# Kernel optimization log

Measured on AMD Instinct MI355X. Metric: run time of the kernel, lower is better.

Reference implementation:

```python
import jax, jax.numpy as jnp
import numpy as np


def setup_inputs() -> dict:
    key = jax.random.key(0)
    k1, k2, k3, k4, k5 = jax.random.split(key, 5)
    B, N, D, H = 4, 1024, 128, 64
    return {
        "embeddings": jax.random.normal(k1, (B, N, D), dtype=jnp.float32),
        "W1": jax.random.normal(k2, (2 * D, H), dtype=jnp.float32) * 0.05,  # Linear(2D -> 64), x@W layout
        "b1": jax.random.normal(k3, (H,), dtype=jnp.float32) * 0.05,
        "W2": jax.random.normal(k4, (H, 1), dtype=jnp.float32) * 0.05,      # Linear(64 -> 1)
        "b2": jax.random.normal(k5, (1,), dtype=jnp.float32) * 0.05,
    }


def reference(embeddings, W1, b1, W2, b2):
    # Original: cat([e_i, e_j]) @ W1 == e_i @ W1[:D] + e_j @ W1[D:]
    # so we compute per-node projections and broadcast-sum, never forming
    # the (B,N,N,2D) concat tensor. Same math, far less traffic.
    B, N, D = embeddings.shape
    Wa, Wb = W1[:D], W1[D:]                      # each (D, 64)
    h_i = jnp.einsum("bnd,dh->bnh", embeddings, Wa)   # (B,N,64)
    h_j = jnp.einsum("bnd,dh->bnh", embeddings, Wb)   # (B,N,64)
    h = jax.nn.relu(h_i[:, :, None, :] + h_j[:, None, :, :] + b1)  # (B,N,N,64)
    scores = jnp.tanh(jnp.einsum("bijh,ho->bijo", h, W2)[..., 0] + b2[0])  # (B,N,N)
    scores = (scores + jnp.swapaxes(scores, 1, 2)) * 0.5  # symmetrize
    return -scores  # complementarity
```

## Files before the change

### kernel.cpp

```cpp
#include <hip/hip_runtime.h>

#define Bb 4
#define Nn 1024
#define Dd 128
#define Hh 64
#define NT 32
#define NPAIRS 528

__device__ __forceinline__ float fast_tanh(float x) {
    const float e = __expf(2.0f * x);
    return __fdividef(e - 1.0f, e + 1.0f);
}

__device__ __forceinline__ int swz_idx(int row, int cw) {
    return row * Hh + (cw ^ (((row >> 2) & 7) << 2));
}

__global__ __launch_bounds__(256) void proj_kernel(
    const float* __restrict__ emb, const float* __restrict__ W1,
    const float* __restrict__ b1, float* __restrict__ HI2, float* __restrict__ HJ)
{
    __shared__ float se[16][132];
    const int tid = threadIdx.x;
    const int row0 = blockIdx.x * 16;
    for (int l = tid; l < 512; l += 256) {
        const int r = l >> 5;
        const int c = l & 31;
        const float4 v = *(const float4*)(emb + (size_t)(row0 + r) * Dd + c * 4);
        *(float4*)&se[r][c * 4] = v;
    }
    __syncthreads();
    const int r  = tid >> 4;
    const int h4 = (tid & 15) * 4;
    float4 acc1 = *(const float4*)(b1 + h4);
    float4 acc2 = make_float4(0.f, 0.f, 0.f, 0.f);
    const float* er = se[r];
    #pragma unroll 4
    for (int d = 0; d < Dd; ++d) {
        const float ev = er[d];
        const float4 wa = *(const float4*)(W1 + (size_t)d * Hh + h4);
        const float4 wb = *(const float4*)(W1 + (size_t)(d + Dd) * Hh + h4);
        acc1.x = fmaf(ev, wa.x, acc1.x); acc1.y = fmaf(ev, wa.y, acc1.y);
        acc1.z = fmaf(ev, wa.z, acc1.z); acc1.w = fmaf(ev, wa.w, acc1.w);
        acc2.x = fmaf(ev, wb.x, acc2.x); acc2.y = fmaf(ev, wb.y, acc2.y);
        acc2.z = fmaf(ev, wb.z, acc2.z); acc2.w = fmaf(ev, wb.w, acc2.w);
    }
    *(float4*)(HI2 + (size_t)(row0 + r) * Hh + h4) = acc1;
    *(float4*)(HJ  + (size_t)(row0 + r) * Hh + h4) = acc2;
}

__global__ __launch_bounds__(256, 4) void score_kernel(
    const float* __restrict__ HI2, const float* __restrict__ HJ,
    const float* __restrict__ W2, const float* __restrict__ b2p,
    float* __restrict__ out)
{
    __shared__ float sAi[32 * Hh];
    __shared__ float sBi[32 * Hh];
    __shared__ float sAj[32 * Hh];
    __shared__ float sBj[32 * Hh];
    __shared__ float sW[Hh];

    const int tid = threadIdx.x;
    const int blk = blockIdx.x;
    const int b = blk / NPAIRS;
    const int p = blk - b * NPAIRS;
    int ti = 0, accum = 0;
    while (accum + (NT - ti) <= p) { accum += NT - ti; ++ti; }
    const int tj = ti + (p - accum);
    const int ri0 = ti * 32, rj0 = tj * 32;

    const float* HIb = HI2 + (size_t)b * Nn * Hh;
    const float* HJb = HJ  + (size_t)b * Nn * Hh;

    if (tid < Hh) sW[tid] = W2[tid];
    for (int l = tid; l < 2048; l += 256) {
        const int which = l >> 9;
        const int rem   = l & 511;
        const int row   = rem >> 4;
        const int cw    = (rem & 15) * 4;
        const float* src;
        float* dst;
        if (which == 0)      { src = HIb + (size_t)(ri0 + row) * Hh; dst = sAi; }
        else if (which == 1) { src = HJb + (size_t)(ri0 + row) * Hh; dst = sBi; }
        else if (which == 2) { src = HIb + (size_t)(rj0 + row) * Hh; dst = sAj; }
        else                 { src = HJb + (size_t)(rj0 + row) * Hh; dst = sBj; }
        const float4 v = *(const float4*)(src + cw);
        *(float4*)&dst[swz_idx(row, cw)] = v;
    }
    __syncthreads();

    const int tx = tid & 15;
    const int ty = tid >> 4;

    float s_ij[2][2] = {{0.f, 0.f}, {0.f, 0.f}};
    float s_ji[2][2] = {{0.f, 0.f}, {0.f, 0.f}};

    for (int hc = 0; hc < 16; ++hc) {
        const int cw = hc * 4;
        const float4 w = *(const float4*)(sW + cw);
        float4 ai[2], bi[2], aj[2], bj[2];
        #pragma unroll
        for (int r = 0; r < 2; ++r) {
            ai[r] = *(const float4*)&sAi[swz_idx(ty * 2 + r, cw)];
            bi[r] = *(const float4*)&sBi[swz_idx(ty * 2 + r, cw)];
        }
        #pragma unroll
        for (int c = 0; c < 2; ++c) {
            aj[c] = *(const float4*)&sAj[swz_idx(tx * 2 + c, cw)];
            bj[c] = *(const float4*)&sBj[swz_idx(tx * 2 + c, cw)];
        }
        #pragma unroll
        for (int r = 0; r < 2; ++r) {
            #pragma unroll
            for (int c = 0; c < 2; ++c) {
                float t;
                t = fmaxf(ai[r].x + bj[c].x, 0.f); s_ij[r][c] = fmaf(t, w.x, s_ij[r][c]);
                t = fmaxf(ai[r].y + bj[c].y, 0.f); s_ij[r][c] = fmaf(t, w.y, s_ij[r][c]);
                t = fmaxf(ai[r].z + bj[c].z, 0.f); s_ij[r][c] = fmaf(t, w.z, s_ij[r][c]);
                t = fmaxf(ai[r].w + bj[c].w, 0.f); s_ij[r][c] = fmaf(t, w.w, s_ij[r][c]);
                t = fmaxf(aj[c].x + bi[r].x, 0.f); s_ji[r][c] = fmaf(t, w.x, s_ji[r][c]);
                t = fmaxf(aj[c].y + bi[r].y, 0.f); s_ji[r][c] = fmaf(t, w.y, s_ji[r][c]);
                t = fmaxf(aj[c].z + bi[r].z, 0.f); s_ji[r][c] = fmaf(t, w.z, s_ji[r][c]);
                t = fmaxf(aj[c].w + bi[r].w, 0.f); s_ji[r][c] = fmaf(t, w.w, s_ji[r][c]);
            }
        }
    }

    const float bb = b2p[0];
    float vals[2][2];
    #pragma unroll
    for (int r = 0; r < 2; ++r)
        #pragma unroll
        for (int c = 0; c < 2; ++c)
            vals[r][c] = -0.5f * (fast_tanh(s_ij[r][c] + bb) + fast_tanh(s_ji[r][c] + bb));

    float* outb = out + (size_t)b * Nn * Nn;
    const int i0 = ri0 + ty * 2;
    const int j0 = rj0 + tx * 2;
    #pragma unroll
    for (int r = 0; r < 2; ++r)
        *(float2*)(outb + (size_t)(i0 + r) * Nn + j0) = make_float2(vals[r][0], vals[r][1]);
    #pragma unroll
    for (int c = 0; c < 2; ++c)
        *(float2*)(outb + (size_t)(j0 + c) * Nn + i0) = make_float2(vals[0][c], vals[1][c]);
}

extern "C" void kernel_launch(void* const* d_in, const int* in_sizes, int n_in,
                              void* d_out, int out_size, void* d_ws, size_t ws_size,
                              hipStream_t stream) {
    const float* emb = (const float*)d_in[0];
    const float* W1  = (const float*)d_in[1];
    const float* b1  = (const float*)d_in[2];
    const float* W2  = (const float*)d_in[3];
    const float* b2  = (const float*)d_in[4];
    float* out = (float*)d_out;
    float* HI2 = (float*)d_ws;
    float* HJ  = HI2 + (size_t)Bb * Nn * Hh;

    proj_kernel<<<(Bb * Nn) / 16, 256, 0, stream>>>(emb, W1, b1, HI2, HJ);
    score_kernel<<<Bb * NPAIRS, 256, 0, stream>>>(HI2, HJ, W2, b2, out);
}
```

Baseline: 106.0 us.

## Enlarge score tiles to 64x64 with 4x4 per-thread outputs and split hidden dim

The score kernel now covers 64x64 tile pairs (136 per batch instead of 528), and each thread computes a 4x4 block of both orientations. The hidden dimension is staged through shared memory in two halves of 32 so shared memory stays the same size. Each loaded row is reused more per shared-memory read, which cuts LDS traffic and per-block overhead, and the output stores widen to float4. In exchange there are fewer blocks (544), higher register pressure with occupancy hint 2, and an extra barrier per phase. The projection kernel also moves to 512 threads, each computing two outputs.

After: 196.0 us. +84.9%, slower.

```diff
diff --git a/kernel.cpp b/kernel.cpp
--- a/kernel.cpp
+++ b/kernel.cpp
@@ -4,145 +4,157 @@
 #define Nn 1024
 #define Dd 128
 #define Hh 64
-#define NT 32
-#define NPAIRS 528
+#define NT2 16
+#define NPAIRS2 136
 
 __device__ __forceinline__ float fast_tanh(float x) {
     const float e = __expf(2.0f * x);
     return __fdividef(e - 1.0f, e + 1.0f);
 }
 
-__device__ __forceinline__ int swz_idx(int row, int cw) {
-    return row * Hh + (cw ^ (((row >> 2) & 7) << 2));
+__device__ __forceinline__ int swz32(int row, int cw) {
+    return row * 32 + (cw ^ (((row >> 2) & 7) << 2));
 }
 
-__global__ __launch_bounds__(256) void proj_kernel(
+__global__ __launch_bounds__(512) void proj_kernel(
     const float* __restrict__ emb, const float* __restrict__ W1,
     const float* __restrict__ b1, float* __restrict__ HI2, float* __restrict__ HJ)
 {
     __shared__ float se[16][132];
     const int tid = threadIdx.x;
     const int row0 = blockIdx.x * 16;
-    for (int l = tid; l < 512; l += 256) {
-        const int r = l >> 5;
-        const int c = l & 31;
+    {
+        const int r = tid >> 5;
+        const int c = tid & 31;
         const float4 v = *(const float4*)(emb + (size_t)(row0 + r) * Dd + c * 4);
         *(float4*)&se[r][c * 4] = v;
     }
     __syncthreads();
-    const int r  = tid >> 4;
-    const int h4 = (tid & 15) * 4;
-    float4 acc1 = *(const float4*)(b1 + h4);
-    float4 acc2 = make_float4(0.f, 0.f, 0.f, 0.f);
+    const int r  = tid >> 5;
+    const int h2 = (tid & 31) * 2;
+    float2 acc1 = *(const float2*)(b1 + h2);
+    float2 acc2 = make_float2(0.f, 0.f);
     const float* er = se[r];
-    #pragma unroll 4
+    #pragma unroll 8
     for (int d = 0; d < Dd; ++d) {
         const float ev = er[d];
-        const float4 wa = *(const float4*)(W1 + (size_t)d * Hh + h4);
-        const float4 wb = *(const float4*)(W1 + (size_t)(d + Dd) * Hh + h4);
+        const float2 wa = *(const float2*)(W1 + (size_t)d * Hh + h2);
+        const float2 wb = *(const float2*)(W1 + (size_t)(d + Dd) * Hh + h2);
         acc1.x = fmaf(ev, wa.x, acc1.x); acc1.y = fmaf(ev, wa.y, acc1.y);
-        acc1.z = fmaf(ev, wa.z, acc1.z); acc1.w = fmaf(ev, wa.w, acc1.w);
         acc2.x = fmaf(ev, wb.x, acc2.x); acc2.y = fmaf(ev, wb.y, acc2.y);
-        acc2.z = fmaf(ev, wb.z, acc2.z); acc2.w = fmaf(ev, wb.w, acc2.w);
     }
-    *(float4*)(HI2 + (size_t)(row0 + r) * Hh + h4) = acc1;
-    *(float4*)(HJ  + (size_t)(row0 + r) * Hh + h4) = acc2;
+    *(float2*)(HI2 + (size_t)(row0 + r) * Hh + h2) = acc1;
+    *(float2*)(HJ  + (size_t)(row0 + r) * Hh + h2) = acc2;
 }
 
-__global__ __launch_bounds__(256, 4) void score_kernel(
+__global__ __launch_bounds__(256, 2) void score_kernel(
     const float* __restrict__ HI2, const float* __restrict__ HJ,
     const float* __restrict__ W2, const float* __restrict__ b2p,
     float* __restrict__ out)
 {
-    __shared__ float sAi[32 * Hh];
-    __shared__ float sBi[32 * Hh];
-    __shared__ float sAj[32 * Hh];
-    __shared__ float sBj[32 * Hh];
+    __shared__ float sAi[64 * 32];
+    __shared__ float sBi[64 * 32];
+    __shared__ float sAj[64 * 32];
+    __shared__ float sBj[64 * 32];
     __shared__ float sW[Hh];
 
     const int tid = threadIdx.x;
     const int blk = blockIdx.x;
-    const int b = blk / NPAIRS;
-    const int p = blk - b * NPAIRS;
+    const int b = blk / NPAIRS2;
+    const int p = blk - b * NPAIRS2;
     int ti = 0, accum = 0;
-    while (accum + (NT - ti) <= p) { accum += NT - ti; ++ti; }
+    while (accum + (NT2 - ti) <= p) { accum += NT2 - ti; ++ti; }
     const int tj = ti + (p - accum);
-    const int ri0 = ti * 32, rj0 = tj * 32;
+    const int ri0 = ti * 64, rj0 = tj * 64;
 
     const float* HIb = HI2 + (size_t)b * Nn * Hh;
     const float* HJb = HJ  + (size_t)b * Nn * Hh;
 
     if (tid < Hh) sW[tid] = W2[tid];
-    for (int l = tid; l < 2048; l += 256) {
-        const int which = l >> 9;
-        const int rem   = l & 511;
-        const int row   = rem >> 4;
-        const int cw    = (rem & 15) * 4;
-        const float* src;
-        float* dst;
-        if (which == 0)      { src = HIb + (size_t)(ri0 + row) * Hh; dst = sAi; }
-        else if (which == 1) { src = HJb + (size_t)(ri0 + row) * Hh; dst = sBi; }
-        else if (which == 2) { src = HIb + (size_t)(rj0 + row) * Hh; dst = sAj; }
-        else                 { src = HJb + (size_t)(rj0 + row) * Hh; dst = sBj; }
-        const float4 v = *(const float4*)(src + cw);
-        *(float4*)&dst[swz_idx(row, cw)] = v;
-    }
-    __syncthreads();
 
     const int tx = tid & 15;
     const int ty = tid >> 4;
 
-    float s_ij[2][2] = {{0.f, 0.f}, {0.f, 0.f}};
-    float s_ji[2][2] = {{0.f, 0.f}, {0.f, 0.f}};
+    float s_ij[4][4];
+    float s_ji[4][4];
+    #pragma unroll
+    for (int r = 0; r < 4; ++r)
+        #pragma unroll
+        for (int c = 0; c < 4; ++c) { s_ij[r][c] = 0.f; s_ji[r][c] = 0.f; }
 
-    for (int hc = 0; hc < 16; ++hc) {
-        const int cw = hc * 4;
-        const float4 w = *(const float4*)(sW + cw);
-        float4 ai[2], bi[2], aj[2], bj[2];
+    for (int ph = 0; ph < 2; ++ph) {
+        if (ph) __syncthreads();
+        const int h0 = ph * 32;
+        for (int l = tid; l < 2048; l += 256) {
+            const int which = l >> 9;
+            const int rem   = l & 511;
+            const int row   = rem >> 3;
+            const int cw    = (rem & 7) * 4;
+            const float* src;
+            float* dst;
+            if (which == 0)      { src = HIb + (size_t)(ri0 + row) * Hh; dst = sAi; }
+            else if (which == 1) { src = HJb + (size_t)(ri0 + row) * Hh; dst = sBi; }
+            else if (which == 2) { src = HIb + (size_t)(rj0 + row) * Hh; dst = sAj; }
+            else                 { src = HJb + (size_t)(rj0 + row) * Hh; dst = sBj; }
+            const float4 v = *(const float4*)(src + h0 + cw);
+            *(float4*)&dst[swz32(row, cw)] = v;
+        }
+        __syncthreads();
+
         #pragma unroll
-        for (int r = 0; r < 2; ++r) {
-            ai[r] = *(const float4*)&sAi[swz_idx(ty * 2 + r, cw)];
-            bi[r] = *(const float4*)&sBi[swz_idx(ty * 2 + r, cw)];
-        }
-        #pragma unroll
-        for (int c = 0; c < 2; ++c) {
-            aj[c] = *(const float4*)&sAj[swz_idx(tx * 2 + c, cw)];
-            bj[c] = *(const float4*)&sBj[swz_idx(tx * 2 + c, cw)];
-        }
-        #pragma unroll
-        for (int r = 0; r < 2; ++r) {
+        for (int hc = 0; hc < 8; ++hc) {
+            const int cw = hc * 4;
+            const float4 w = *(const float4*)(sW + h0 + cw);
+            float4 ai[4], bi[4], aj[4], bj[4];
             #pragma unroll
-            for (int c = 0; c < 2; ++c) {
-                float t;
-                t = fmaxf(ai[r].x + bj[c].x, 0.f); s_ij[r][c] = fmaf(t, w.x, s_ij[r][c]);
-                t = fmaxf(ai[r].y + bj[c].y, 0.f); s_ij[r][c] = fmaf(t, w.y, s_ij[r][c]);
-                t = fmaxf(ai[r].z + bj[c].z, 0.f); s_ij[r][c] = fmaf(t, w.z, s_ij[r][c]);
-                t = fmaxf(ai[r].w + bj[c].w, 0.f); s_ij[r][c] = fmaf(t, w.w, s_ij[r][c]);
-                t = fmaxf(aj[c].x + bi[r].x, 0.f); s_ji[r][c] = fmaf(t, w.x, s_ji[r][c]);
-                t = fmaxf(aj[c].y + bi[r].y, 0.f); s_ji[r][c] = fmaf(t, w.y, s_ji[r][c]);
-                t = fmaxf(aj[c].z + bi[r].z, 0.f); s_ji[r][c] = fmaf(t, w.z, s_ji[r][c]);
-                t = fmaxf(aj[c].w + bi[r].w, 0.f); s_ji[r][c] = fmaf(t, w.w, s_ji[r][c]);
+            for (int r = 0; r < 4; ++r) {
+                ai[r] = *(const float4*)&sAi[swz32(ty * 4 + r, cw)];
+                bi[r] = *(const float4*)&sBi[swz32(ty * 4 + r, cw)];
+            }
+            #pragma unroll
+            for (int c = 0; c < 4; ++c) {
+                aj[c] = *(const float4*)&sAj[swz32(tx * 4 + c, cw)];
+                bj[c] = *(const float4*)&sBj[swz32(tx * 4 + c, cw)];
+            }
+            #pragma unroll
+            for (int r = 0; r < 4; ++r) {
+                #pragma unroll
+                for (int c = 0; c < 4; ++c) {
+                    float t;
+                    t = fmaxf(ai[r].x + bj[c].x, 0.f); s_ij[r][c] = fmaf(t, w.x, s_ij[r][c]);
+                    t = fmaxf(ai[r].y + bj[c].y, 0.f); s_ij[r][c] = fmaf(t, w.y, s_ij[r][c]);
+                    t = fmaxf(ai[r].z + bj[c].z, 0.f); s_ij[r][c] = fmaf(t, w.z, s_ij[r][c]);
+                    t = fmaxf(ai[r].w + bj[c].w, 0.f); s_ij[r][c] = fmaf(t, w.w, s_ij[r][c]);
+                    t = fmaxf(aj[c].x + bi[r].x, 0.f); s_ji[r][c] = fmaf(t, w.x, s_ji[r][c]);
+                    t = fmaxf(aj[c].y + bi[r].y, 0.f); s_ji[r][c] = fmaf(t, w.y, s_ji[r][c]);
+                    t = fmaxf(aj[c].z + bi[r].z, 0.f); s_ji[r][c] = fmaf(t, w.z, s_ji[r][c]);
+                    t = fmaxf(aj[c].w + bi[r].w, 0.f); s_ji[r][c] = fmaf(t, w.w, s_ji[r][c]);
+                }
             }
         }
     }
 
     const float bb = b2p[0];
-    float vals[2][2];
+    float vals[4][4];
     #pragma unroll
-    for (int r = 0; r < 2; ++r)
+    for (int r = 0; r < 4; ++r)
         #pragma unroll
-        for (int c = 0; c < 2; ++c)
+        for (int c = 0; c < 4; ++c)
             vals[r][c] = -0.5f * (fast_tanh(s_ij[r][c] + bb) + fast_tanh(s_ji[r][c] + bb));
 
     float* outb = out + (size_t)b * Nn * Nn;
-    const int i0 = ri0 + ty * 2;
-    const int j0 = rj0 + tx * 2;
+    const int i0 = ri0 + ty * 4;
+    const int j0 = rj0 + tx * 4;
     #pragma unroll
-    for (int r = 0; r < 2; ++r)
-        *(float2*)(outb + (size_t)(i0 + r) * Nn + j0) = make_float2(vals[r][0], vals[r][1]);
+    for (int r = 0; r < 4; ++r) {
+        float4 v = make_float4(vals[r][0], vals[r][1], vals[r][2], vals[r][3]);
+        *(float4*)(outb + (size_t)(i0 + r) * Nn + j0) = v;
+    }
     #pragma unroll
-    for (int c = 0; c < 2; ++c)
-        *(float2*)(outb + (size_t)(j0 + c) * Nn + i0) = make_float2(vals[0][c], vals[1][c]);
+    for (int c = 0; c < 4; ++c) {
+        float4 v = make_float4(vals[0][c], vals[1][c], vals[2][c], vals[3][c]);
+        *(float4*)(outb + (size_t)(j0 + c) * Nn + i0) = v;
+    }
 }
 
 extern "C" void kernel_launch(void* const* d_in, const int* in_sizes, int n_in,
@@ -157,6 +169,6 @@
     float* HI2 = (float*)d_ws;
     float* HJ  = HI2 + (size_t)Bb * Nn * Hh;
 
-    proj_kernel<<<(Bb * Nn) / 16, 256, 0, stream>>>(emb, W1, b1, HI2, HJ);
-    score_kernel<<<Bb * NPAIRS, 256, 0, stream>>>(HI2, HJ, W2, b2, out);
+    proj_kernel<<<(Bb * Nn) / 16, 512, 0, stream>>>(emb, W1, b1, HI2, HJ);
+    score_kernel<<<Bb * NPAIRS2, 256, 0, stream>>>(HI2, HJ, W2, b2, out);
 }
```
